# Optimization experiments

Measured on AMD Instinct MI355X. Metric: run time of the kernel, lower is better.

## Reference

```python
import jax, jax.numpy as jnp
import numpy as np

SEQ, D, H, DH = 118, 128, 4, 32
NEG = -1e9


def _rope_tables():
    # matches the second (overwriting) computation in __init__: base=10000, dim=128
    ch = jnp.arange(0, D, 2, dtype=jnp.float32)
    inv_freq = 1.0 / (10000.0 ** (ch / D))
    t = jnp.arange(SEQ, dtype=jnp.float32)
    freqs = jnp.outer(t, inv_freq)                      # (118, 64)
    return jnp.cos(freqs).astype(jnp.bfloat16), jnp.sin(freqs).astype(jnp.bfloat16)


def _apply_rope(x, cos, sin):
    # x: (b, 118, 128); cos/sin: (118, 64) bf16 -> promote to f32 in the mul
    d = x.shape[-1] // 2
    x1, x2 = x[..., :d], x[..., d:]
    y1 = x1 * cos + x2 * sin
    y2 = -x1 * sin + x2 * cos
    return jnp.concatenate([y1, y2], axis=-1).astype(x.dtype)


def _layernorm(x, g, b, eps=1e-5):
    mu = jnp.mean(x, -1, keepdims=True)
    var = jnp.mean(jnp.square(x - mu), -1, keepdims=True)
    return (x - mu) * jax.lax.rsqrt(var + eps) * g + b


def _attention_block(x, qkv_w, qkv_b, fc2_w, fc2_b, cos, sin, mask):
    b = x.shape[0]
    qkv = x @ qkv_w.T + qkv_b                           # (b, 118, 384)
    q, k, v = jnp.split(qkv, 3, axis=-1)
    q = _apply_rope(q, cos, sin)
    k = _apply_rope(k, cos, sin)
    # faithful to view(b,118,32,4) + rearrange 'b l d h -> b h l d'
    to_heads = lambda t: jnp.transpose(t.reshape(b, SEQ, DH, H), (0, 3, 1, 2))
    q, k, v = to_heads(q), to_heads(k), to_heads(v)     # (b, 4, 118, 32)
    scores = jnp.einsum('bhqd,bhkd->bhqk', q, k) / jnp.sqrt(jnp.float32(DH))
    scores = jnp.where(mask, scores, NEG)
    attn = jax.nn.softmax(scores, axis=-1)
    y = jnp.einsum('bhqk,bhkd->bhqd', attn, v)          # (b, 4, 118, 32)
    y = jnp.transpose(y, (0, 2, 1, 3)).reshape(b, SEQ, D)
    return jax.nn.silu(y @ fc2_w.T + fc2_b)


def setup_inputs() -> dict:
    key = jax.random.key(0)
    ks = jax.random.split(key, 10)
    s = lambda fan_in: 1.0 / np.sqrt(fan_in)
    inp = {
        'x': jax.random.normal(ks[0], (8192, SEQ), jnp.float32),
        'fc1_w': jax.random.uniform(ks[1], (D, 1), jnp.float32, -1.0, 1.0),
        'fc1_b': jax.random.uniform(ks[2], (D,), jnp.float32, -1.0, 1.0),
        'qkv_w': jax.random.uniform(ks[3], (3 * D, D), jnp.float32, -s(D), s(D)),
        'qkv_b': jax.random.uniform(ks[4], (3 * D,), jnp.float32, -s(D), s(D)),
        'fc2_w': jax.random.uniform(ks[5], (D, D), jnp.float32, -s(D), s(D)),
        'fc2_b': jax.random.uniform(ks[6], (D,), jnp.float32, -s(D), s(D)),
        'fc3_w': jax.random.uniform(ks[7], (1, D), jnp.float32, -s(D), s(D)),
        'fc3_b': jax.random.uniform(ks[8], (1,), jnp.float32, -s(D), s(D)),
        'ln_g': jnp.ones((D,), jnp.float32),
        'ln_b': jnp.zeros((D,), jnp.float32),
    }
    return inp


def reference(x, fc1_w, fc1_b, qkv_w, qkv_b, fc2_w, fc2_b, fc3_w, fc3_b, ln_g, ln_b):
    cos, sin = _rope_tables()
    mask = jnp.tril(jnp.ones((SEQ, SEQ), dtype=bool))
    h = jax.nn.silu(x[..., None] @ fc1_w.T + fc1_b)     # (b, 118, 128)
    x1 = _attention_block(h, qkv_w, qkv_b, fc2_w, fc2_b, cos, sin, mask)
    x2 = x1 + _attention_block(_layernorm(x1, ln_g, ln_b), qkv_w, qkv_b, fc2_w, fc2_b, cos, sin, mask)
    return (x2 @ fc3_w.T + fc3_b).squeeze(-1)           # (b, 118)
```

## Files before the change

### kernel.cpp

```cpp
#include <hip/hip_runtime.h>
#include <hip/hip_bf16.h>

#define SEQ 118
#define YS  136
#define SQS 40
#define SVS 136

typedef __attribute__((ext_vector_type(8))) short short8;
typedef __attribute__((ext_vector_type(4))) float f32x4;

__device__ __forceinline__ f32x4 mfma16(short8 a, short8 b, f32x4 c){
  return __builtin_amdgcn_mfma_f32_16x16x32_bf16(a, b, c, 0, 0, 0);
}
__device__ __forceinline__ float bfr(float x){
  return __bfloat162float(__float2bfloat16(x));
}
__device__ __forceinline__ float rcpf(float x){ return __builtin_amdgcn_rcpf(x); }
__device__ __forceinline__ float fsilu(float z){
  return z * rcpf(1.f + exp2f(-1.442695041f * z));
}
__device__ __forceinline__ float rsum16(float v){
  v += __shfl_xor(v,1); v += __shfl_xor(v,2); v += __shfl_xor(v,4); v += __shfl_xor(v,8);
  return v;
}
__device__ __forceinline__ float rmax16(float v){
  v = fmaxf(v, __shfl_xor(v,1)); v = fmaxf(v, __shfl_xor(v,2));
  v = fmaxf(v, __shfl_xor(v,4)); v = fmaxf(v, __shfl_xor(v,8));
  return v;
}
__device__ __forceinline__ unsigned pack_bf2(float lo, float hi){
  __hip_bfloat162 h2 = __float22bfloat162_rn(float2{lo, hi});
  unsigned u; __builtin_memcpy(&u, &h2, 4);
  return u;
}

__global__ void prep_kernel(const float* __restrict__ qkv_w,
                            const float* __restrict__ fc2_w,
                            __hip_bfloat16* __restrict__ wbf){
  int i = blockIdx.x * 256 + threadIdx.x;
  int seg = i >> 14;
  int r   = i & 16383;
  int row = r >> 7;
  int k   = r & 127;
  float v;
  if (seg < 3){
    int h = row >> 5, n = row & 31;
    v = qkv_w[(seg*128 + 4*n + h)*128 + k];
  } else {
    int h = k >> 5, rr = k & 31;
    int dh = (rr >> 1) + (rr & 1)*16;
    v = fc2_w[row*128 + h*32 + dh];
  }
  wbf[i] = __float2bfloat16(v);
}

__launch_bounds__(512, 4)
__global__ void fused_kernel(const float* __restrict__ x,
                             const float* __restrict__ fc1_w, const float* __restrict__ fc1_b,
                             const float* __restrict__ qkv_b,
                             const float* __restrict__ fc2_b, const float* __restrict__ fc3_w,
                             const float* __restrict__ fc3_b,
                             const float* __restrict__ ln_g,  const float* __restrict__ ln_b,
                             const __hip_bfloat16* __restrict__ wbf,
                             float* __restrict__ out)
{
  __shared__ __align__(16) char smem[63328];
  __hip_bfloat16* Ybuf = (__hip_bfloat16*)(smem);
  __hip_bfloat16* sQP  = (__hip_bfloat16*)(smem + 32096);
  __hip_bfloat16* sK   = (__hip_bfloat16*)(smem + 42336);
  __hip_bfloat16* sVt  = (__hip_bfloat16*)(smem + 52576);
  float*          sCb  = (float*)        (smem + 61280);

  const __hip_bfloat16* wq  = wbf;
  const __hip_bfloat16* wk  = wbf + 16384;
  const __hip_bfloat16* wvw = wbf + 32768;
  const __hip_bfloat16* w2  = wbf + 49152;

  const int b    = blockIdx.x;
  const int tid  = threadIdx.x;
  const int wv   = tid >> 6;
  const int lane = tid & 63;
  const int c    = lane & 15;
  const int quad = lane >> 4;
  const int arow = wv*16 + c;

  {
    int i = tid;
    if (i < 512){
      float v;
      if      (i < 128) v = fc2_b[i];
      else if (i < 256) v = fc3_w[i-128];
      else if (i < 384) v = ln_g [i-256];
      else              v = ln_b [i-384];
      sCb[i] = v;
    }
  }
  __syncthreads();

  float o1[4];

  #pragma unroll 1
  for (int p = 0; p < 2; ++p){
    short8 afr[4];
    if (p == 0){
      float xs = (arow < SEQ) ? x[b*SEQ + arow] : 0.f;
      #pragma unroll
      for (int k4 = 0; k4 < 4; k4++){
        int d0 = k4*32 + quad*8;
        short8 fr;
        #pragma unroll
        for (int i = 0; i < 8; i++){
          float z = xs * fc1_w[d0+i] + fc1_b[d0+i];
          float v = fsilu(z);
          if (arow >= SEQ) v = 0.f;
          fr[i] = (short)__builtin_bit_cast(unsigned short, __float2bfloat16(v));
        }
        afr[k4] = fr;
      }
    } else {
      #pragma unroll
      for (int k4 = 0; k4 < 4; k4++){
        short8 fr = *(const short8*)(Ybuf + arow*YS + k4*32 + quad*8);
        if (arow >= SEQ) fr = (short8){0,0,0,0,0,0,0,0};
        afr[k4] = fr;
      }
    }

    #pragma unroll 1
    for (int h = 0; h < 4; ++h){
      const float invf = exp2f((float)(4*c + h) * (-0.20762050593045f));

      {
        const __hip_bfloat16* wpq = wq + (h*32 + c)*128 + quad*8;
        const __hip_bfloat16* wpk = wk + (h*32 + c)*128 + quad*8;
        f32x4 q0={0,0,0,0}, q1={0,0,0,0}, k0={0,0,0,0}, k1={0,0,0,0};
        #pragma unroll
        for (int k4 = 0; k4 < 4; k4++){
          short8 bq0 = *(const short8*)(wpq + k4*32);
          short8 bq1 = *(const short8*)(wpq + 2048 + k4*32);
          short8 bk0 = *(const short8*)(wpk + k4*32);
          short8 bk1 = *(const short8*)(wpk + 2048 + k4*32);
          q0 = mfma16(afr[k4], bq0, q0);
          q1 = mfma16(afr[k4], bq1, q1);
          k0 = mfma16(afr[k4], bk0, k0);
          k1 = mfma16(afr[k4], bk1, k1);
        }
        const float KSC = 0.25500526963f;
        float bQ0 = qkv_b[      4*c + h], bQ1 = qkv_b[ 64 + 4*c + h];
        float bK0 = qkv_b[128 + 4*c + h], bK1 = qkv_b[192 + 4*c + h];
        #pragma unroll
        for (int j = 0; j < 4; j++){
          int s = wv*16 + quad*4 + j;
          float ang = (float)s * invf;
          float cv = bfr(__cosf(ang)), sv = bfr(__sinf(ang));
          float cvq = cv*KSC, svq = sv*KSC;
          float xq1 = q0[j] + bQ0, xq2 = q1[j] + bQ1;
          float xk1 = k0[j] + bK0, xk2 = k1[j] + bK1;
          *(unsigned*)(sQP + s*SQS + 2*c) = pack_bf2( xq1*cvq + xq2*svq, -xq1*svq + xq2*cvq);
          *(unsigned*)(sK  + s*SQS + 2*c) = pack_bf2( xk1*cv  + xk2*sv , -xk1*sv  + xk2*cv );
        }
      }
      {
        const __hip_bfloat16* wpv = wvw + (h*32 + c)*128 + quad*8;
        f32x4 v0={0,0,0,0}, v1={0,0,0,0};
        #pragma unroll
        for (int k4 = 0; k4 < 4; k4++){
          short8 b0 = *(const short8*)(wpv + k4*32);
          short8 b1 = *(const short8*)(wpv + 2048 + k4*32);
          v0 = mfma16(afr[k4], b0, v0);
          v1 = mfma16(afr[k4], b1, v1);
        }
        float bV0 = qkv_b[256 + 4*c + h], bV1 = qkv_b[320 + 4*c + h];
        int s0 = wv*16 + quad*4;
        *(unsigned*)(sVt + (c   )*SVS + s0    ) = pack_bf2(v0[0]+bV0, v0[1]+bV0);
        *(unsigned*)(sVt + (c   )*SVS + s0 + 2) = pack_bf2(v0[2]+bV0, v0[3]+bV0);
        *(unsigned*)(sVt + (c+16)*SVS + s0    ) = pack_bf2(v1[0]+bV1, v1[1]+bV1);
        *(unsigned*)(sVt + (c+16)*SVS + s0 + 2) = pack_bf2(v1[2]+bV1, v1[3]+bV1);
      }
      __syncthreads();

      short8 aq = *(const short8*)(sQP + arow*SQS + quad*8);
      f32x4 sc[8];
      #pragma unroll
      for (int t = 0; t < 8; t++){
        sc[t] = (f32x4){0.f,0.f,0.f,0.f};
        if (t <= wv){
          short8 bk = *(const short8*)(sK + (t*16 + c)*SQS + quad*8);
          f32x4 z = {0,0,0,0};
          sc[t] = mfma16(aq, bk, z);
        }
      }
      float rnorm[4];
      #pragma unroll
      for (int j = 0; j < 4; j++){
        float mx = -3.0e38f;
        #pragma unroll
        for (int t = 0; t < 8; t++){
          if (t < wv){
            mx = fmaxf(mx, sc[t][j]);
          } else if (t == wv){
            float v = (c <= quad*4 + j) ? sc[t][j] : -1.0e9f;
            sc[t][j] = v;
            mx = fmaxf(mx, v);
          }
        }
        mx = rmax16(mx);
        float sum = 0.f;
        #pragma unroll
        for (int t = 0; t < 8; t++) if (t <= wv){
          float e = exp2f(sc[t][j] - mx); sc[t][j] = e; sum += e;
        }
        sum = rsum16(sum);
        rnorm[j] = rcpf(sum);
      }

      f32x4 y0 = {0,0,0,0}, y1 = {0,0,0,0};
      auto pv_quarter = [&](int qt, f32x4 pa, f32x4 pb){
        int s0 = wv*16 + quad*4;
        #pragma unroll
        for (int j = 0; j < 4; j++){
          sQP[(s0+j)*SQS + c     ] = __float2bfloat16(pa[j]);
          sQP[(s0+j)*SQS + 16 + c] = __float2bfloat16(pb[j]);
        }
        short8 ap  = *(const short8*)(sQP + arow*SQS + quad*8);
        short8 bv0 = *(const short8*)(sVt + (c   )*SVS + qt*32 + quad*8);
        short8 bv1 = *(const short8*)(sVt + (c+16)*SVS + qt*32 + quad*8);
        y0 = mfma16(ap, bv0, y0);
        y1 = mfma16(ap, bv1, y1);
      };
      int qmax = wv >> 1;
      pv_quarter(0, sc[0], sc[1]);
      if (qmax >= 1) pv_quarter(1, sc[2], sc[3]);
      if (qmax >= 2) pv_quarter(2, sc[4], sc[5]);
      if (qmax >= 3) pv_quarter(3, sc[6], sc[7]);
      #pragma unroll
      for (int j = 0; j < 4; j++){ y0[j] *= rnorm[j]; y1[j] *= rnorm[j]; }

      {
        int s0 = wv*16 + quad*4;
        #pragma unroll
        for (int j = 0; j < 4; j++)
          if (s0 + j < SEQ)
            *(unsigned*)(Ybuf + (s0+j)*YS + h*32 + 2*c) = pack_bf2(y0[j], y1[j]);
      }
      __syncthreads();
    }

    short8 ay[4];
    #pragma unroll
    for (int k4 = 0; k4 < 4; k4++)
      ay[k4] = *(const short8*)(Ybuf + arow*YS + k4*32 + quad*8);
    f32x4 xx[8];
    f32x4 S1 = {0,0,0,0}, S2 = {0,0,0,0}, S3 = {0,0,0,0};
    #pragma unroll 1
    for (int t = 0; t < 8; t++){
      f32x4 acc = {0,0,0,0};
      #pragma unroll
      for (int k4 = 0; k4 < 4; k4++){
        short8 bw = *(const short8*)(w2 + (t*16 + c)*128 + k4*32 + quad*8);
        acc = mfma16(ay[k4], bw, acc);
      }
      float bias = sCb[t*16 + c];
      float w3   = sCb[128 + t*16 + c];
      #pragma unroll
      for (int j = 0; j < 4; j++){
        float v = fsilu(acc[j] + bias);
        xx[t][j] = v;
        S1[j] += v; S2[j] += v*v; S3[j] += v*w3;
      }
    }
    #pragma unroll
    for (int j = 0; j < 4; j++){
      float s1 = rsum16(S1[j]), s2 = rsum16(S2[j]), s3 = rsum16(S3[j]);
      int s = wv*16 + quad*4 + j;
      if (p == 0){
        float mu  = s1 * (1.f/128.f);
        float var = fmaxf(s2 * (1.f/128.f) - mu*mu, 0.f);
        float rs  = rsqrtf(var + 1e-5f);
        if (s < SEQ){
          #pragma unroll
          for (int t = 0; t < 8; t++){
            int d = t*16 + c;
            Ybuf[s*YS + d] = __float2bfloat16((xx[t][j] - mu)*rs*sCb[256+d] + sCb[384+d]);
          }
        }
        o1[j] = s3;
      } else {
        if (c == 0 && s < SEQ) out[b*SEQ + s] = o1[j] + s3 + fc3_b[0];
      }
    }
    if (p == 0) __syncthreads();
  }
}

extern "C" void kernel_launch(void* const* d_in, const int* in_sizes, int n_in,
                              void* d_out, int out_size, void* d_ws, size_t ws_size,
                              hipStream_t stream){
  const float* x     = (const float*)d_in[0];
  const float* fc1_w = (const float*)d_in[1];
  const float* fc1_b = (const float*)d_in[2];
  const float* qkv_w = (const float*)d_in[3];
  const float* qkv_b = (const float*)d_in[4];
  const float* fc2_w = (const float*)d_in[5];
  const float* fc2_b = (const float*)d_in[6];
  const float* fc3_w = (const float*)d_in[7];
  const float* fc3_b = (const float*)d_in[8];
  const float* ln_g  = (const float*)d_in[9];
  const float* ln_b  = (const float*)d_in[10];

  __hip_bfloat16* wbf = (__hip_bfloat16*)d_ws;
  prep_kernel<<<256, 256, 0, stream>>>(qkv_w, fc2_w, wbf);

  const int B = in_sizes[0] / SEQ;
  fused_kernel<<<B, 512, 0, stream>>>(x, fc1_w, fc1_b, qkv_b, fc2_b, fc3_w, fc3_b,
                                      ln_g, ln_b, wbf, (float*)d_out);
}
```

Before: 2.521 ms.

## Swizzle shared buffers, shrink LDS, alternate causal row mapping, raise occupancy

```diff
diff --git a/kernel.cpp b/kernel.cpp
--- a/kernel.cpp
+++ b/kernel.cpp
@@ -2,9 +2,7 @@
 #include <hip/hip_bf16.h>
 
 #define SEQ 118
-#define YS  136
-#define SQS 40
-#define SVS 136
+#define SQS 32
 
 typedef __attribute__((ext_vector_type(8))) short short8;
 typedef __attribute__((ext_vector_type(4))) float f32x4;
@@ -32,6 +30,9 @@
   __hip_bfloat162 h2 = __float22bfloat162_rn(float2{lo, hi});
   unsigned u; __builtin_memcpy(&u, &h2, 4);
   return u;
+}
+__device__ __forceinline__ int yadr(int row, int col){
+  return row*128 + ((((col >> 3) ^ (row & 15)) << 3) | (col & 7));
 }
 
 __global__ void prep_kernel(const float* __restrict__ qkv_w,
@@ -54,7 +55,7 @@
   wbf[i] = __float2bfloat16(v);
 }
 
-__launch_bounds__(512, 4)
+__launch_bounds__(512, 6)
 __global__ void fused_kernel(const float* __restrict__ x,
                              const float* __restrict__ fc1_w, const float* __restrict__ fc1_b,
                              const float* __restrict__ qkv_b,
@@ -64,12 +65,11 @@
                              const __hip_bfloat16* __restrict__ wbf,
                              float* __restrict__ out)
 {
-  __shared__ __align__(16) char smem[63328];
+  __shared__ __align__(16) char smem[54144];
   __hip_bfloat16* Ybuf = (__hip_bfloat16*)(smem);
-  __hip_bfloat16* sQP  = (__hip_bfloat16*)(smem + 32096);
-  __hip_bfloat16* sK   = (__hip_bfloat16*)(smem + 42336);
-  __hip_bfloat16* sVt  = (__hip_bfloat16*)(smem + 52576);
-  float*          sCb  = (float*)        (smem + 61280);
+  __hip_bfloat16* sQP  = (__hip_bfloat16*)(smem + 30208);
+  __hip_bfloat16* sK   = (__hip_bfloat16*)(smem + 38400);
+  __hip_bfloat16* sVt  = (__hip_bfloat16*)(smem + 45952);
 
   const __hip_bfloat16* wq  = wbf;
   const __hip_bfloat16* wk  = wbf + 16384;
@@ -84,19 +84,6 @@
   const int quad = lane >> 4;
   const int arow = wv*16 + c;
 
-  {
-    int i = tid;
-    if (i < 512){
-      float v;
-      if      (i < 128) v = fc2_b[i];
-      else if (i < 256) v = fc3_w[i-128];
-      else if (i < 384) v = ln_g [i-256];
-      else              v = ln_b [i-384];
-      sCb[i] = v;
-    }
-  }
-  __syncthreads();
-
   float o1[4];
 
   #pragma unroll 1
@@ -120,8 +107,8 @@
     } else {
       #pragma unroll
       for (int k4 = 0; k4 < 4; k4++){
-        short8 fr = *(const short8*)(Ybuf + arow*YS + k4*32 + quad*8);
-        if (arow >= SEQ) fr = (short8){0,0,0,0,0,0,0,0};
+        short8 fr = (arow < SEQ) ? *(const short8*)(Ybuf + yadr(arow, k4*32 + quad*8))
+                                 : (short8){0,0,0,0,0,0,0,0};
         afr[k4] = fr;
       }
     }
@@ -157,7 +144,8 @@
           float xq1 = q0[j] + bQ0, xq2 = q1[j] + bQ1;
           float xk1 = k0[j] + bK0, xk2 = k1[j] + bK1;
           *(unsigned*)(sQP + s*SQS + 2*c) = pack_bf2( xq1*cvq + xq2*svq, -xq1*svq + xq2*cvq);
-          *(unsigned*)(sK  + s*SQS + 2*c) = pack_bf2( xk1*cv  + xk2*sv , -xk1*sv  + xk2*cv );
+          if (s < SEQ)
+            *(unsigned*)(sK + s*SQS + 2*c) = pack_bf2( xk1*cv + xk2*sv, -xk1*sv + xk2*cv);
         }
       }
       {
@@ -172,19 +160,20 @@
         }
         float bV0 = qkv_b[256 + 4*c + h], bV1 = qkv_b[320 + 4*c + h];
         int s0 = wv*16 + quad*4;
-        *(unsigned*)(sVt + (c   )*SVS + s0    ) = pack_bf2(v0[0]+bV0, v0[1]+bV0);
-        *(unsigned*)(sVt + (c   )*SVS + s0 + 2) = pack_bf2(v0[2]+bV0, v0[3]+bV0);
-        *(unsigned*)(sVt + (c+16)*SVS + s0    ) = pack_bf2(v1[0]+bV1, v1[1]+bV1);
-        *(unsigned*)(sVt + (c+16)*SVS + s0 + 2) = pack_bf2(v1[2]+bV1, v1[3]+bV1);
+        *(unsigned*)(sVt + yadr(c,      s0    )) = pack_bf2(v0[0]+bV0, v0[1]+bV0);
+        *(unsigned*)(sVt + yadr(c,      s0 + 2)) = pack_bf2(v0[2]+bV0, v0[3]+bV0);
+        *(unsigned*)(sVt + yadr(c + 16, s0    )) = pack_bf2(v1[0]+bV1, v1[1]+bV1);
+        *(unsigned*)(sVt + yadr(c + 16, s0 + 2)) = pack_bf2(v1[2]+bV1, v1[3]+bV1);
       }
       __syncthreads();
 
-      short8 aq = *(const short8*)(sQP + arow*SQS + quad*8);
+      const int st = (h & 1) ? (7 - wv) : wv;
+      short8 aq = *(const short8*)(sQP + (st*16 + c)*SQS + quad*8);
       f32x4 sc[8];
       #pragma unroll
       for (int t = 0; t < 8; t++){
         sc[t] = (f32x4){0.f,0.f,0.f,0.f};
-        if (t <= wv){
+        if (t <= st){
           short8 bk = *(const short8*)(sK + (t*16 + c)*SQS + quad*8);
           f32x4 z = {0,0,0,0};
           sc[t] = mfma16(aq, bk, z);
@@ -196,9 +185,9 @@
         float mx = -3.0e38f;
         #pragma unroll
         for (int t = 0; t < 8; t++){
-          if (t < wv){
+          if (t < st){
             mx = fmaxf(mx, sc[t][j]);
-          } else if (t == wv){
+          } else if (t == st){
             float v = (c <= quad*4 + j) ? sc[t][j] : -1.0e9f;
             sc[t][j] = v;
             mx = fmaxf(mx, v);
@@ -207,7 +196,7 @@
         mx = rmax16(mx);
         float sum = 0.f;
         #pragma unroll
-        for (int t = 0; t < 8; t++) if (t <= wv){
+        for (int t = 0; t < 8; t++) if (t <= st){
           float e = exp2f(sc[t][j] - mx); sc[t][j] = e; sum += e;
         }
         sum = rsum16(sum);
@@ -216,19 +205,19 @@
 
       f32x4 y0 = {0,0,0,0}, y1 = {0,0,0,0};
       auto pv_quarter = [&](int qt, f32x4 pa, f32x4 pb){
-        int s0 = wv*16 + quad*4;
+        int s0 = st*16 + quad*4;
         #pragma unroll
         for (int j = 0; j < 4; j++){
           sQP[(s0+j)*SQS + c     ] = __float2bfloat16(pa[j]);
           sQP[(s0+j)*SQS + 16 + c] = __float2bfloat16(pb[j]);
         }
-        short8 ap  = *(const short8*)(sQP + arow*SQS + quad*8);
-        short8 bv0 = *(const short8*)(sVt + (c   )*SVS + qt*32 + quad*8);
-        short8 bv1 = *(const short8*)(sVt + (c+16)*SVS + qt*32 + quad*8);
+        short8 ap  = *(const short8*)(sQP + (st*16 + c)*SQS + quad*8);
+        short8 bv0 = *(const short8*)(sVt + yadr(c,      qt*32 + quad*8));
+        short8 bv1 = *(const short8*)(sVt + yadr(c + 16, qt*32 + quad*8));
         y0 = mfma16(ap, bv0, y0);
         y1 = mfma16(ap, bv1, y1);
       };
-      int qmax = wv >> 1;
+      int qmax = st >> 1;
       pv_quarter(0, sc[0], sc[1]);
       if (qmax >= 1) pv_quarter(1, sc[2], sc[3]);
       if (qmax >= 2) pv_quarter(2, sc[4], sc[5]);
@@ -237,11 +226,11 @@
       for (int j = 0; j < 4; j++){ y0[j] *= rnorm[j]; y1[j] *= rnorm[j]; }
 
       {
-        int s0 = wv*16 + quad*4;
+        int s0 = st*16 + quad*4;
         #pragma unroll
         for (int j = 0; j < 4; j++)
           if (s0 + j < SEQ)
-            *(unsigned*)(Ybuf + (s0+j)*YS + h*32 + 2*c) = pack_bf2(y0[j], y1[j]);
+            *(unsigned*)(Ybuf + yadr(s0 + j, h*32 + 2*c)) = pack_bf2(y0[j], y1[j]);
       }
       __syncthreads();
     }
@@ -249,7 +238,8 @@
     short8 ay[4];
     #pragma unroll
     for (int k4 = 0; k4 < 4; k4++)
-      ay[k4] = *(const short8*)(Ybuf + arow*YS + k4*32 + quad*8);
+      ay[k4] = (arow < SEQ) ? *(const short8*)(Ybuf + yadr(arow, k4*32 + quad*8))
+                            : (short8){0,0,0,0,0,0,0,0};
     f32x4 xx[8];
     f32x4 S1 = {0,0,0,0}, S2 = {0,0,0,0}, S3 = {0,0,0,0};
     #pragma unroll 1
@@ -260,8 +250,8 @@
         short8 bw = *(const short8*)(w2 + (t*16 + c)*128 + k4*32 + quad*8);
         acc = mfma16(ay[k4], bw, acc);
       }
-      float bias = sCb[t*16 + c];
-      float w3   = sCb[128 + t*16 + c];
+      float bias = fc2_b[t*16 + c];
+      float w3   = fc3_w[t*16 + c];
       #pragma unroll
       for (int j = 0; j < 4; j++){
         float v = fsilu(acc[j] + bias);
@@ -281,7 +271,7 @@
           #pragma unroll
           for (int t = 0; t < 8; t++){
             int d = t*16 + c;
-            Ybuf[s*YS + d] = __float2bfloat16((xx[t][j] - mu)*rs*sCb[256+d] + sCb[384+d]);
+            Ybuf[yadr(s, d)] = __float2bfloat16((xx[t][j] - mu)*rs*ln_g[d] + ln_b[d]);
           }
         }
         o1[j] = s3;
```

New measurement: 4.057 ms. +60.9%, slower.
